# Kernel tuning notes

Hardware: AMD Instinct MI355X
Metric: run time of the kernel (lower is better)

## Reference

```python
import jax, jax.numpy as jnp
import numpy as np

K = 3
STRIDE = 1
PAD = 1
IN_CH = 64
OUT_CH = 128
ALPHA = 0.5  # scaling_factor
QMAX = 127.0  # 8-bit symmetric fake quant


def fake_quant(x):
    # per-tensor symmetric 8-bit fake quant with dynamic amax + STE
    amax = jnp.max(jnp.abs(jax.lax.stop_gradient(x)))
    s = jnp.where(amax > 0, amax / QMAX, 1.0)
    q = jnp.clip(jnp.round(x / s), -QMAX, QMAX) * s
    return x + jax.lax.stop_gradient(q - x)


def im2col(x, k, stride, pad):
    # x: (B, C, H, W) -> (B, C*k*k, h_out*w_out), torch.nn.functional.unfold order (C slowest, then kh, kw)
    B, C, H, W = x.shape
    h_out = (H + 2 * pad - k) // stride + 1
    w_out = (W + 2 * pad - k) // stride + 1
    xp = jnp.pad(x, ((0, 0), (0, 0), (pad, pad), (pad, pad)))
    patches = [xp[:, :, i:i + stride * h_out:stride, j:j + stride * w_out:stride]
               for i in range(k) for j in range(k)]  # fixed k*k loop
    cols = jnp.stack(patches, axis=2)  # (B, C, k*k, h_out, w_out)
    return cols.reshape(B, C * k * k, h_out * w_out), h_out, w_out


def setup_inputs() -> dict:
    key = jax.random.key(0)
    k1, k2 = jax.random.split(key)
    inp = jax.random.normal(k1, (16, IN_CH, 128, 128), dtype=jnp.float32)
    weight = jax.random.normal(k2, (OUT_CH, IN_CH, K, K), dtype=jnp.float32) * 0.05
    return {"input": inp, "weight": weight}


def reference(input, weight):
    bs = input.shape[0]
    ksize = IN_CH * K * K
    cols, h_out, w_out = im2col(input, K, STRIDE, PAD)  # (B, ksize, L)
    num_sliding = cols.shape[2]
    x = jnp.transpose(cols, (0, 2, 1)).reshape(-1, ksize)  # (B*L, ksize)
    w_flat = weight.reshape(OUT_CH, ksize)

    act_scale = jnp.max(jnp.abs(jax.lax.stop_gradient(x)), axis=0)       # (ksize,)
    weight_scale = jnp.max(jnp.abs(jax.lax.stop_gradient(w_flat)), axis=0)  # (ksize,)
    scale = act_scale ** ALPHA / weight_scale ** (1.0 - ALPHA)
    scale = jnp.where(scale == 0, 1.0, scale)

    x = fake_quant(x / scale)
    w_flat = fake_quant(w_flat * scale)

    out = jnp.einsum('nk,ok->no', x, w_flat)  # (B*L, OUT_CH)
    out = out.reshape(bs, num_sliding, OUT_CH)
    out = jnp.transpose(out, (0, 2, 1)).reshape(bs, OUT_CH, h_out, w_out)
    return out
```

## Files before the change

### kernel.cpp

```cpp
#include <hip/hip_runtime.h>

#define BATCH 16
#define CIN   64
#define HW    128
#define OC    128
#define KSIZE 576

typedef float float4v __attribute__((ext_vector_type(4)));
typedef int   int4v   __attribute__((ext_vector_type(4)));
typedef unsigned int uint;

#define WS_ACT   0
#define WS_WSC   576
#define WS_XMUL  1152
#define WS_SXSW  1728
#define WS_WQ_BYTE_OFF 8192

#define SWZ(x) ((((x) & 3) ^ (((x) >> 2) & 3)))
#define MAGIC 12582912.0f

__device__ __forceinline__ void async_cp16(const void* g, void* l) {
    __builtin_amdgcn_global_load_lds(
        (const __attribute__((address_space(1))) unsigned int*)g,
        (__attribute__((address_space(3))) unsigned int*)l, 16, 0, 0);
}

__global__ __launch_bounds__(256) void k_absmax(const float* __restrict__ in,
                                                const float* __restrict__ w,
                                                float* __restrict__ wsf) {
    const int tid = threadIdx.x, lane = tid & 63, wid = tid >> 6;
    if (blockIdx.x < 1024) {
        const int c = blockIdx.x >> 4, bs = blockIdx.x & 15;
        const float4v* p = (const float4v*)(in + (size_t)(bs * CIN + c) * (HW * HW));
        float m[9];
#pragma unroll
        for (int i = 0; i < 9; ++i) m[i] = 0.f;
        for (int e = tid; e < 4096; e += 256) {
            const int h = e >> 5, q = e & 31;
            const float4v v = p[e];
            const float a0 = fabsf(v[0]), a1 = fabsf(v[1]), a2 = fabsf(v[2]), a3 = fabsf(v[3]);
            const float m01 = fmaxf(a0, a1), m12 = fmaxf(a1, a2);
            const float mall = fmaxf(m01, fmaxf(a2, a3));
            const float mw0 = (q == 31) ? fmaxf(m01, a2) : mall;
            const float mw2 = (q == 0)  ? fmaxf(m12, a3) : mall;
            const bool h0 = (h <= 126), h2 = (h >= 1);
            m[0] = fmaxf(m[0], h0 ? mw0 : 0.f);
            m[1] = fmaxf(m[1], h0 ? mall : 0.f);
            m[2] = fmaxf(m[2], h0 ? mw2 : 0.f);
            m[3] = fmaxf(m[3], mw0);
            m[4] = fmaxf(m[4], mall);
            m[5] = fmaxf(m[5], mw2);
            m[6] = fmaxf(m[6], h2 ? mw0 : 0.f);
            m[7] = fmaxf(m[7], h2 ? mall : 0.f);
            m[8] = fmaxf(m[8], h2 ? mw2 : 0.f);
        }
#pragma unroll
        for (int i = 0; i < 9; ++i)
            for (int off = 32; off; off >>= 1)
                m[i] = fmaxf(m[i], __shfl_down(m[i], off));
        __shared__ float sred[4][9];
        if (lane == 0)
#pragma unroll
            for (int i = 0; i < 9; ++i) sred[wid][i] = m[i];
        __syncthreads();
        if (tid < 9) {
            float mm = fmaxf(fmaxf(sred[0][tid], sred[1][tid]),
                             fmaxf(sred[2][tid], sred[3][tid]));
            atomicMax((int*)(wsf + WS_ACT + c * 9 + tid), __float_as_int(mm));
        }
    } else {
        const int k = (blockIdx.x - 1024) * 4 + wid;
        float m = fmaxf(fabsf(w[lane * KSIZE + k]), fabsf(w[(lane + 64) * KSIZE + k]));
        for (int off = 32; off; off >>= 1) m = fmaxf(m, __shfl_down(m, off));
        if (lane == 0) wsf[WS_WSC + k] = m;
    }
}

__global__ __launch_bounds__(576) void k_scale_wq(const float* __restrict__ w,
                                                  float* __restrict__ wsf,
                                                  char* __restrict__ wq_s) {
    __shared__ float ls[576];
    __shared__ float redA[9], redB[9];
    const int t = threadIdx.x, o = blockIdx.x;
    const int lane = t & 63, wid = t >> 6;
    const float a = wsf[WS_ACT + t];
    const float wv = wsf[WS_WSC + t];
    float s = sqrtf(a) / sqrtf(wv);
    if (s == 0.f) s = 1.f;
    ls[t] = s;
    float v1 = a / s;
    float v2 = wv * s;
    for (int off = 32; off; off >>= 1) {
        v1 = fmaxf(v1, __shfl_down(v1, off));
        v2 = fmaxf(v2, __shfl_down(v2, off));
    }
    if (lane == 0) { redA[wid] = v1; redB[wid] = v2; }
    __syncthreads();
    float ax = redA[0], aw = redB[0];
#pragma unroll
    for (int i = 1; i < 9; ++i) { ax = fmaxf(ax, redA[i]); aw = fmaxf(aw, redB[i]); }
    const float sx = ax > 0.f ? ax / 127.f : 1.f;
    const float sw = aw > 0.f ? aw / 127.f : 1.f;
    const int r = t >> 6, c = t & 63, ko = c * 9 + r;
    float q = rintf((w[o * KSIZE + ko] * ls[ko]) / sw);
    q = fminf(127.f, fmaxf(-127.f, q));
    const int qi = (int)q;
    const int fc = c >> 4;
    wq_s[r * 8192 + o * 64 + ((fc ^ SWZ(o)) << 4) + (c & 15)] = (char)qi;
    if (o == 0) {
        wsf[WS_XMUL + t] = 1.0f / (ls[ko] * sx);
        if (t == 0) wsf[WS_SXSW] = sx * sw;
    }
}

__global__ __launch_bounds__(512, 4) void k_gemm(const float* __restrict__ in,
                                                 const char* __restrict__ wq_s,
                                                 const float* __restrict__ wsf,
                                                 float* __restrict__ out) {
    __shared__ int4v Bl4[4608];
    __shared__ float xml[576];
    char* Bl = (char*)Bl4;

    const int tid = threadIdx.x, lane = tid & 63, w = tid >> 6;
    const int xcd = blockIdx.x & 7, idx = blockIdx.x >> 3;
    const int ohp = idx & 7;
    const int b = idx >> 3;
    const int wh = w >> 2, wm = w & 3;
    const int oh = xcd * 16 + ohp * 2 + wh;
    const int l15 = lane & 15, fsel = lane >> 4;
    const int ow0 = wm * 32 + l15;

#pragma unroll
    for (int i = 0; i < 9; ++i)
        async_cp16(wq_s + i * 8192 + tid * 16, Bl + i * 8192 + tid * 16);
    if (tid < 144)
        ((float4v*)xml)[tid] = ((const float4v*)(wsf + WS_XMUL))[tid];
    __syncthreads();

    const float* pb = in + ((size_t)b * CIN + fsel * 16) * (HW * HW);

    int4v acc0[8], acc1[8];
#pragma unroll
    for (int nt = 0; nt < 8; ++nt) {
        acc0[nt] = (int4v){0, 0, 0, 0};
        acc1[nt] = (int4v){0, 0, 0, 0};
    }

#pragma unroll
    for (int r = 0; r < 9; ++r) {
        const int kh = r / 3, kw = r - 3 * kh;
        const int h = oh + kh - 1;
        if (h >= 0 && h < HW) {
            const int iw0 = ow0 + kw - 1;
            const int iw1 = iw0 + 16;
            int iwc0 = iw0, iwc1 = iw1;
            if (kw == 0) iwc0 = iw0 < 0 ? 0 : iw0;
            if (kw == 2) iwc1 = iw1 > 127 ? 127 : iw1;
            const float* p0 = pb + h * HW + iwc0;
            const float* p1 = pb + h * HW + iwc1;
            float v0[16], v1[16];
#pragma unroll
            for (int j = 0; j < 16; ++j) {
                v0[j] = p0[j * (HW * HW)];
                v1[j] = p1[j * (HW * HW)];
            }
            const float* xp = xml + r * 64 + (fsel << 4);
            uint pk0[4], pk1[4];
#pragma unroll
            for (int d = 0; d < 4; ++d) {
                const float4v xq = *(const float4v*)(xp + d * 4);
                uint u0[4], u1[4];
#pragma unroll
                for (int j2 = 0; j2 < 4; ++j2) {
                    u0[j2] = __float_as_uint(fmaf(v0[d * 4 + j2], xq[j2], MAGIC));
                    u1[j2] = __float_as_uint(fmaf(v1[d * 4 + j2], xq[j2], MAGIC));
                }
                const uint a01 = __builtin_amdgcn_perm(u0[1], u0[0], 0x0C0C0400u);
                const uint a23 = __builtin_amdgcn_perm(u0[3], u0[2], 0x0C0C0400u);
                pk0[d] = __builtin_amdgcn_perm(a23, a01, 0x05040100u);
                const uint b01 = __builtin_amdgcn_perm(u1[1], u1[0], 0x0C0C0400u);
                const uint b23 = __builtin_amdgcn_perm(u1[3], u1[2], 0x0C0C0400u);
                pk1[d] = __builtin_amdgcn_perm(b23, b01, 0x05040100u);
            }
            int4v af0, af1;
            if (kw == 0) {
                const uint msk = ((unsigned)iw0 < 128u) ? 0xFFFFFFFFu : 0u;
                af0 = (int4v){(int)(pk0[0] & msk), (int)(pk0[1] & msk),
                              (int)(pk0[2] & msk), (int)(pk0[3] & msk)};
                af1 = (int4v){(int)pk1[0], (int)pk1[1], (int)pk1[2], (int)pk1[3]};
            } else if (kw == 2) {
                const uint msk = ((unsigned)iw1 < 128u) ? 0xFFFFFFFFu : 0u;
                af0 = (int4v){(int)pk0[0], (int)pk0[1], (int)pk0[2], (int)pk0[3]};
                af1 = (int4v){(int)(pk1[0] & msk), (int)(pk1[1] & msk),
                              (int)(pk1[2] & msk), (int)(pk1[3] & msk)};
            } else {
                af0 = (int4v){(int)pk0[0], (int)pk0[1], (int)pk0[2], (int)pk0[3]};
                af1 = (int4v){(int)pk1[0], (int)pk1[1], (int)pk1[2], (int)pk1[3]};
            }
#pragma unroll
            for (int nt = 0; nt < 8; ++nt) {
                const int br = nt * 16 + l15;
                const int4v bf = *(const int4v*)(Bl + r * 8192 + br * 64 +
                                                 ((fsel ^ SWZ(br)) << 4));
                acc0[nt] = __builtin_amdgcn_mfma_i32_16x16x64_i8(af0, bf, acc0[nt], 0, 0, 0);
                acc1[nt] = __builtin_amdgcn_mfma_i32_16x16x64_i8(af1, bf, acc1[nt], 0, 0, 0);
            }
        }
    }

    const float sxsw = wsf[WS_SXSW];
    const int owp = wm * 32 + (fsel << 2);
#pragma unroll
    for (int nt = 0; nt < 8; ++nt) {
        const int o = nt * 16 + l15;
        float4v rv0, rv1;
#pragma unroll
        for (int q = 0; q < 4; ++q) {
            rv0[q] = (float)acc0[nt][q] * sxsw;
            rv1[q] = (float)acc1[nt][q] * sxsw;
        }
        float* po = out + ((size_t)(b * OC + o) * HW + oh) * HW;
        *(float4v*)(po + owp) = rv0;
        *(float4v*)(po + owp + 16) = rv1;
    }
}

extern "C" void kernel_launch(void* const* d_in, const int* in_sizes, int n_in,
                              void* d_out, int out_size, void* d_ws, size_t ws_size,
                              hipStream_t stream) {
    const float* in = (const float*)d_in[0];
    const float* wt = (const float*)d_in[1];
    float* out = (float*)d_out;
    float* wsf = (float*)d_ws;
    char* wq_s = (char*)d_ws + WS_WQ_BYTE_OFF;

    k_absmax<<<dim3(1024 + 144), dim3(256), 0, stream>>>(in, wt, wsf);
    k_scale_wq<<<dim3(128), dim3(576), 0, stream>>>(wt, wsf, wq_s);
    k_gemm<<<dim3(BATCH * HW / 2), dim3(512), 0, stream>>>(in, wq_s, wsf, out);
}
```

Before: 222.3 us.

## Build all activation fragments before the barrier, then run MFMAs per output-tile pair

The loop is restructured so that all nine kernel-position activation fragments are loaded, quantized and packed into registers first. The barrier moves after this phase, so the async weight-to-LDS copy overlaps with the global loads and quantization. MFMAs then run over output-channel pairs with a smaller accumulator set, and each pair's results are stored as soon as it finishes. Out-of-bounds rows are handled with clamped addresses plus masks instead of a branch, and the scale vector is read from global memory instead of LDS. Holding 18 fragment vectors raises register pressure, and edge rows now issue loads that are thrown away.

```diff
diff --git a/kernel.cpp b/kernel.cpp
--- a/kernel.cpp
+++ b/kernel.cpp
@@ -118,7 +118,6 @@
                                                  const float* __restrict__ wsf,
                                                  float* __restrict__ out) {
     __shared__ int4v Bl4[4608];
-    __shared__ float xml[576];
     char* Bl = (char*)Bl4;
 
     const int tid = threadIdx.x, lane = tid & 63, w = tid >> 6;
@@ -133,95 +132,92 @@
 #pragma unroll
     for (int i = 0; i < 9; ++i)
         async_cp16(wq_s + i * 8192 + tid * 16, Bl + i * 8192 + tid * 16);
-    if (tid < 144)
-        ((float4v*)xml)[tid] = ((const float4v*)(wsf + WS_XMUL))[tid];
-    __syncthreads();
 
     const float* pb = in + ((size_t)b * CIN + fsel * 16) * (HW * HW);
-
-    int4v acc0[8], acc1[8];
-#pragma unroll
-    for (int nt = 0; nt < 8; ++nt) {
-        acc0[nt] = (int4v){0, 0, 0, 0};
-        acc1[nt] = (int4v){0, 0, 0, 0};
-    }
-
+    const float* xmg = wsf + WS_XMUL;
+
+    int4v af0[9], af1[9];
 #pragma unroll
     for (int r = 0; r < 9; ++r) {
         const int kh = r / 3, kw = r - 3 * kh;
         const int h = oh + kh - 1;
-        if (h >= 0 && h < HW) {
-            const int iw0 = ow0 + kw - 1;
-            const int iw1 = iw0 + 16;
-            int iwc0 = iw0, iwc1 = iw1;
-            if (kw == 0) iwc0 = iw0 < 0 ? 0 : iw0;
-            if (kw == 2) iwc1 = iw1 > 127 ? 127 : iw1;
-            const float* p0 = pb + h * HW + iwc0;
-            const float* p1 = pb + h * HW + iwc1;
-            float v0[16], v1[16];
-#pragma unroll
-            for (int j = 0; j < 16; ++j) {
-                v0[j] = p0[j * (HW * HW)];
-                v1[j] = p1[j * (HW * HW)];
+        const int hc = h < 0 ? 0 : (h > 127 ? 127 : h);
+        const bool hok = (h >= 0) & (h < 128);
+        const int iw0 = ow0 + kw - 1;
+        const int iw1 = iw0 + 16;
+        int iwc0 = iw0, iwc1 = iw1;
+        if (kw == 0) iwc0 = iw0 < 0 ? 0 : iw0;
+        if (kw == 2) iwc1 = iw1 > 127 ? 127 : iw1;
+        const float* p0 = pb + hc * HW + iwc0;
+        const float* p1 = pb + hc * HW + iwc1;
+        float v0[16], v1[16];
+#pragma unroll
+        for (int j = 0; j < 16; ++j) {
+            v0[j] = p0[j * (HW * HW)];
+            v1[j] = p1[j * (HW * HW)];
+        }
+        uint pk0[4], pk1[4];
+#pragma unroll
+        for (int d = 0; d < 4; ++d) {
+            const float4v xq = *(const float4v*)(xmg + r * 64 + (fsel << 4) + d * 4);
+            uint u0[4], u1[4];
+#pragma unroll
+            for (int j2 = 0; j2 < 4; ++j2) {
+                u0[j2] = __float_as_uint(fmaf(v0[d * 4 + j2], xq[j2], MAGIC));
+                u1[j2] = __float_as_uint(fmaf(v1[d * 4 + j2], xq[j2], MAGIC));
             }
-            const float* xp = xml + r * 64 + (fsel << 4);
-            uint pk0[4], pk1[4];
-#pragma unroll
-            for (int d = 0; d < 4; ++d) {
-                const float4v xq = *(const float4v*)(xp + d * 4);
-                uint u0[4], u1[4];
-#pragma unroll
-                for (int j2 = 0; j2 < 4; ++j2) {
-                    u0[j2] = __float_as_uint(fmaf(v0[d * 4 + j2], xq[j2], MAGIC));
-                    u1[j2] = __float_as_uint(fmaf(v1[d * 4 + j2], xq[j2], MAGIC));
-                }
-                const uint a01 = __builtin_amdgcn_perm(u0[1], u0[0], 0x0C0C0400u);
-                const uint a23 = __builtin_amdgcn_perm(u0[3], u0[2], 0x0C0C0400u);
-                pk0[d] = __builtin_amdgcn_perm(a23, a01, 0x05040100u);
-                const uint b01 = __builtin_amdgcn_perm(u1[1], u1[0], 0x0C0C0400u);
-                const uint b23 = __builtin_amdgcn_perm(u1[3], u1[2], 0x0C0C0400u);
-                pk1[d] = __builtin_amdgcn_perm(b23, b01, 0x05040100u);
-            }
-            int4v af0, af1;
-            if (kw == 0) {
-                const uint msk = ((unsigned)iw0 < 128u) ? 0xFFFFFFFFu : 0u;
-                af0 = (int4v){(int)(pk0[0] & msk), (int)(pk0[1] & msk),
-                              (int)(pk0[2] & msk), (int)(pk0[3] & msk)};
-                af1 = (int4v){(int)pk1[0], (int)pk1[1], (int)pk1[2], (int)pk1[3]};
-            } else if (kw == 2) {
-                const uint msk = ((unsigned)iw1 < 128u) ? 0xFFFFFFFFu : 0u;
-                af0 = (int4v){(int)pk0[0], (int)pk0[1], (int)pk0[2], (int)pk0[3]};
-                af1 = (int4v){(int)(pk1[0] & msk), (int)(pk1[1] & msk),
-                              (int)(pk1[2] & msk), (int)(pk1[3] & msk)};
-            } else {
-                af0 = (int4v){(int)pk0[0], (int)pk0[1], (int)pk0[2], (int)pk0[3]};
-                af1 = (int4v){(int)pk1[0], (int)pk1[1], (int)pk1[2], (int)pk1[3]};
-            }
-#pragma unroll
-            for (int nt = 0; nt < 8; ++nt) {
-                const int br = nt * 16 + l15;
-                const int4v bf = *(const int4v*)(Bl + r * 8192 + br * 64 +
-                                                 ((fsel ^ SWZ(br)) << 4));
-                acc0[nt] = __builtin_amdgcn_mfma_i32_16x16x64_i8(af0, bf, acc0[nt], 0, 0, 0);
-                acc1[nt] = __builtin_amdgcn_mfma_i32_16x16x64_i8(af1, bf, acc1[nt], 0, 0, 0);
-            }
-        }
-    }
+            const uint a01 = __builtin_amdgcn_perm(u0[1], u0[0], 0x0C0C0400u);
+            const uint a23 = __builtin_amdgcn_perm(u0[3], u0[2], 0x0C0C0400u);
+            pk0[d] = __builtin_amdgcn_perm(a23, a01, 0x05040100u);
+            const uint b01 = __builtin_amdgcn_perm(u1[1], u1[0], 0x0C0C0400u);
+            const uint b23 = __builtin_amdgcn_perm(u1[3], u1[2], 0x0C0C0400u);
+            pk1[d] = __builtin_amdgcn_perm(b23, b01, 0x05040100u);
+        }
+        uint m0 = hok ? 0xFFFFFFFFu : 0u;
+        uint m1 = m0;
+        if (kw == 0) { if (!((unsigned)iw0 < 128u)) m0 = 0u; }
+        if (kw == 2) { if (!((unsigned)iw1 < 128u)) m1 = 0u; }
+        af0[r] = (int4v){(int)(pk0[0] & m0), (int)(pk0[1] & m0),
+                         (int)(pk0[2] & m0), (int)(pk0[3] & m0)};
+        af1[r] = (int4v){(int)(pk1[0] & m1), (int)(pk1[1] & m1),
+                         (int)(pk1[2] & m1), (int)(pk1[3] & m1)};
+    }
+
+    __syncthreads();
 
     const float sxsw = wsf[WS_SXSW];
     const int owp = wm * 32 + (fsel << 2);
 #pragma unroll
-    for (int nt = 0; nt < 8; ++nt) {
-        const int o = nt * 16 + l15;
-        float4v rv0, rv1;
-#pragma unroll
-        for (int q = 0; q < 4; ++q) {
-            rv0[q] = (float)acc0[nt][q] * sxsw;
-            rv1[q] = (float)acc1[nt][q] * sxsw;
-        }
-        float* po = out + ((size_t)(b * OC + o) * HW + oh) * HW;
-        *(float4v*)(po + owp) = rv0;
-        *(float4v*)(po + owp + 16) = rv1;
+    for (int p = 0; p < 4; ++p) {
+        int4v acc[4];
+#pragma unroll
+        for (int q = 0; q < 4; ++q) acc[q] = (int4v){0, 0, 0, 0};
+        const int br0 = (2 * p) * 16 + l15;
+        const int br1 = br0 + 16;
+        const int off0 = br0 * 64 + ((fsel ^ SWZ(br0)) << 4);
+        const int off1 = br1 * 64 + ((fsel ^ SWZ(br1)) << 4);
+#pragma unroll
+        for (int r = 0; r < 9; ++r) {
+            const int4v bf0 = *(const int4v*)(Bl + r * 8192 + off0);
+            const int4v bf1 = *(const int4v*)(Bl + r * 8192 + off1);
+            acc[0] = __builtin_amdgcn_mfma_i32_16x16x64_i8(af0[r], bf0, acc[0], 0, 0, 0);
+            acc[1] = __builtin_amdgcn_mfma_i32_16x16x64_i8(af1[r], bf0, acc[1], 0, 0, 0);
+            acc[2] = __builtin_amdgcn_mfma_i32_16x16x64_i8(af0[r], bf1, acc[2], 0, 0, 0);
+            acc[3] = __builtin_amdgcn_mfma_i32_16x16x64_i8(af1[r], bf1, acc[3], 0, 0, 0);
+        }
+#pragma unroll
+        for (int s = 0; s < 2; ++s) {
+            const int o = (2 * p + s) * 16 + l15;
+            float4v rv0, rv1;
+#pragma unroll
+            for (int q = 0; q < 4; ++q) {
+                rv0[q] = (float)acc[2 * s + 0][q] * sxsw;
+                rv1[q] = (float)acc[2 * s + 1][q] * sxsw;
+            }
+            float* po = out + ((size_t)(b * OC + o) * HW + oh) * HW;
+            *(float4v*)(po + owp) = rv0;
+            *(float4v*)(po + owp + 16) = rv1;
+        }
     }
 }
 
```

Result: slower. 250.9 us (+12.9%).

## Software-pipeline activation loads in conv GEMM with register double buffering

Applied to the files above, without the earlier changes.

Restructures the 9-tap loop into 18 half-chunks that prefetch the next tap's 16 activation values into a register buffer while the current half's MFMAs run, and issues the first prefetch before the barrier so it overlaps the async LDS weight copy. Out-of-range rows are now clamped and masked instead of skipped by a branch, so edge rows do extra zero MFMAs. This raises register pressure under the 512-thread, 4-blocks launch bound, which may cause spills.

```diff
diff --git a/kernel.cpp b/kernel.cpp
--- a/kernel.cpp
+++ b/kernel.cpp
@@ -113,6 +113,27 @@
     }
 }
 
+__device__ __forceinline__ const float* a_ptr(const float* pb, int oh, int ow0,
+                                              int R, int F) {
+    const int kh = R / 3, kw = R % 3;
+    int h = oh + kh - 1;
+    h = h < 0 ? 0 : (h > 127 ? 127 : h);
+    int iw = ow0 + (F ? 16 : 0) + kw - 1;
+    if (kw == 0 && F == 0) iw = iw < 0 ? 0 : iw;
+    if (kw == 2 && F == 1) iw = iw > 127 ? 127 : iw;
+    return pb + h * HW + iw;
+}
+
+__device__ __forceinline__ uint a_msk(int oh, int ow0, int R, int F) {
+    const int kh = R / 3, kw = R % 3;
+    const int h = oh + kh - 1;
+    uint m = ((unsigned)h < 128u) ? 0xFFFFFFFFu : 0u;
+    const int iw = ow0 + (F ? 16 : 0) + kw - 1;
+    if ((kw == 0 && F == 0) || (kw == 2 && F == 1))
+        if (!((unsigned)iw < 128u)) m = 0u;
+    return m;
+}
+
 __global__ __launch_bounds__(512, 4) void k_gemm(const float* __restrict__ in,
                                                  const char* __restrict__ wq_s,
                                                  const float* __restrict__ wsf,
@@ -135,9 +156,19 @@
         async_cp16(wq_s + i * 8192 + tid * 16, Bl + i * 8192 + tid * 16);
     if (tid < 144)
         ((float4v*)xml)[tid] = ((const float4v*)(wsf + WS_XMUL))[tid];
-    __syncthreads();
 
     const float* pb = in + ((size_t)b * CIN + fsel * 16) * (HW * HW);
+
+    float vbuf[2][16];
+    {
+        const float* p0 = a_ptr(pb, oh, ow0, 0, 0);
+        const float* p1 = a_ptr(pb, oh, ow0, 0, 1);
+#pragma unroll
+        for (int j = 0; j < 16; ++j) {
+            vbuf[0][j] = p0[j * (HW * HW)];
+            vbuf[1][j] = p1[j * (HW * HW)];
+        }
+    }
 
     int4v acc0[8], acc1[8];
 #pragma unroll
@@ -146,67 +177,58 @@
         acc1[nt] = (int4v){0, 0, 0, 0};
     }
 
-#pragma unroll
-    for (int r = 0; r < 9; ++r) {
-        const int kh = r / 3, kw = r - 3 * kh;
-        const int h = oh + kh - 1;
-        if (h >= 0 && h < HW) {
-            const int iw0 = ow0 + kw - 1;
-            const int iw1 = iw0 + 16;
-            int iwc0 = iw0, iwc1 = iw1;
-            if (kw == 0) iwc0 = iw0 < 0 ? 0 : iw0;
-            if (kw == 2) iwc1 = iw1 > 127 ? 127 : iw1;
-            const float* p0 = pb + h * HW + iwc0;
-            const float* p1 = pb + h * HW + iwc1;
-            float v0[16], v1[16];
-#pragma unroll
-            for (int j = 0; j < 16; ++j) {
-                v0[j] = p0[j * (HW * HW)];
-                v1[j] = p1[j * (HW * HW)];
-            }
-            const float* xp = xml + r * 64 + (fsel << 4);
-            uint pk0[4], pk1[4];
-#pragma unroll
-            for (int d = 0; d < 4; ++d) {
-                const float4v xq = *(const float4v*)(xp + d * 4);
-                uint u0[4], u1[4];
-#pragma unroll
-                for (int j2 = 0; j2 < 4; ++j2) {
-                    u0[j2] = __float_as_uint(fmaf(v0[d * 4 + j2], xq[j2], MAGIC));
-                    u1[j2] = __float_as_uint(fmaf(v1[d * 4 + j2], xq[j2], MAGIC));
-                }
-                const uint a01 = __builtin_amdgcn_perm(u0[1], u0[0], 0x0C0C0400u);
-                const uint a23 = __builtin_amdgcn_perm(u0[3], u0[2], 0x0C0C0400u);
-                pk0[d] = __builtin_amdgcn_perm(a23, a01, 0x05040100u);
-                const uint b01 = __builtin_amdgcn_perm(u1[1], u1[0], 0x0C0C0400u);
-                const uint b23 = __builtin_amdgcn_perm(u1[3], u1[2], 0x0C0C0400u);
-                pk1[d] = __builtin_amdgcn_perm(b23, b01, 0x05040100u);
-            }
-            int4v af0, af1;
-            if (kw == 0) {
-                const uint msk = ((unsigned)iw0 < 128u) ? 0xFFFFFFFFu : 0u;
-                af0 = (int4v){(int)(pk0[0] & msk), (int)(pk0[1] & msk),
-                              (int)(pk0[2] & msk), (int)(pk0[3] & msk)};
-                af1 = (int4v){(int)pk1[0], (int)pk1[1], (int)pk1[2], (int)pk1[3]};
-            } else if (kw == 2) {
-                const uint msk = ((unsigned)iw1 < 128u) ? 0xFFFFFFFFu : 0u;
-                af0 = (int4v){(int)pk0[0], (int)pk0[1], (int)pk0[2], (int)pk0[3]};
-                af1 = (int4v){(int)(pk1[0] & msk), (int)(pk1[1] & msk),
-                              (int)(pk1[2] & msk), (int)(pk1[3] & msk)};
-            } else {
-                af0 = (int4v){(int)pk0[0], (int)pk0[1], (int)pk0[2], (int)pk0[3]};
-                af1 = (int4v){(int)pk1[0], (int)pk1[1], (int)pk1[2], (int)pk1[3]};
-            }
-#pragma unroll
-            for (int nt = 0; nt < 8; ++nt) {
-                const int br = nt * 16 + l15;
-                const int4v bf = *(const int4v*)(Bl + r * 8192 + br * 64 +
-                                                 ((fsel ^ SWZ(br)) << 4));
-                acc0[nt] = __builtin_amdgcn_mfma_i32_16x16x64_i8(af0, bf, acc0[nt], 0, 0, 0);
-                acc1[nt] = __builtin_amdgcn_mfma_i32_16x16x64_i8(af1, bf, acc1[nt], 0, 0, 0);
-            }
-        }
-    }
+    __syncthreads();
+
+#define HALFCHUNK(HC)                                                          \
+    {                                                                          \
+        constexpr int R = (HC) >> 1, F = (HC) & 1;                             \
+        const float* xp = xml + R * 64 + (fsel << 4);                          \
+        uint pk[4];                                                            \
+        _Pragma("unroll")                                                      \
+        for (int d = 0; d < 4; ++d) {                                          \
+            const float4v xq = *(const float4v*)(xp + d * 4);                  \
+            uint u[4];                                                         \
+            _Pragma("unroll")                                                  \
+            for (int j2 = 0; j2 < 4; ++j2)                                     \
+                u[j2] = __float_as_uint(fmaf(vbuf[F][d * 4 + j2], xq[j2], MAGIC)); \
+            const uint p01 = __builtin_amdgcn_perm(u[1], u[0], 0x0C0C0400u);   \
+            const uint p23 = __builtin_amdgcn_perm(u[3], u[2], 0x0C0C0400u);   \
+            pk[d] = __builtin_amdgcn_perm(p23, p01, 0x05040100u);              \
+        }                                                                      \
+        const uint msk = a_msk(oh, ow0, R, F);                                 \
+        const int4v af = (int4v){(int)(pk[0] & msk), (int)(pk[1] & msk),       \
+                                 (int)(pk[2] & msk), (int)(pk[3] & msk)};      \
+        if ((HC) + 2 < 18) {                                                   \
+            const float* pn = a_ptr(pb, oh, ow0, ((HC) + 2) >> 1, F);          \
+            _Pragma("unroll")                                                  \
+            for (int j = 0; j < 16; ++j) vbuf[F][j] = pn[j * (HW * HW)];       \
+        }                                                                      \
+        if (F == 0) {                                                          \
+            _Pragma("unroll")                                                  \
+            for (int nt = 0; nt < 8; ++nt) {                                   \
+                const int br = nt * 16 + l15;                                  \
+                const int4v bf = *(const int4v*)(Bl + R * 8192 + br * 64 +     \
+                                                 ((fsel ^ SWZ(br)) << 4));     \
+                acc0[nt] = __builtin_amdgcn_mfma_i32_16x16x64_i8(af, bf,       \
+                                                          acc0[nt], 0, 0, 0); \
+            }                                                                  \
+        } else {                                                               \
+            _Pragma("unroll")                                                  \
+            for (int nt = 0; nt < 8; ++nt) {                                   \
+                const int br = nt * 16 + l15;                                  \
+                const int4v bf = *(const int4v*)(Bl + R * 8192 + br * 64 +     \
+                                                 ((fsel ^ SWZ(br)) << 4));     \
+                acc1[nt] = __builtin_amdgcn_mfma_i32_16x16x64_i8(af, bf,       \
+                                                          acc1[nt], 0, 0, 0); \
+            }                                                                  \
+        }                                                                      \
+    }
+
+    HALFCHUNK(0)  HALFCHUNK(1)  HALFCHUNK(2)  HALFCHUNK(3)  HALFCHUNK(4)
+    HALFCHUNK(5)  HALFCHUNK(6)  HALFCHUNK(7)  HALFCHUNK(8)  HALFCHUNK(9)
+    HALFCHUNK(10) HALFCHUNK(11) HALFCHUNK(12) HALFCHUNK(13) HALFCHUNK(14)
+    HALFCHUNK(15) HALFCHUNK(16) HALFCHUNK(17)
+#undef HALFCHUNK
 
     const float sxsw = wsf[WS_SXSW];
     const int owp = wm * 32 + (fsel << 2);
```

Measured after the change: 437.8 us. 1.97x slower.

## Load each input row once per kh and derive kw shifts via lane shuffles

Applied to the files above, without the earlier changes.

The GEMM kernel now loads the 32 input columns for each kernel row once and builds the left and right shifted tap operands with cross-lane shuffles inside 16-lane groups. Halo columns come from a separate per-lane load that is broadcast with shuffles. This cuts global/L2 loads by about a factor of three. In exchange it adds many shuffle (ds_bpermute/DPP) instructions and selects per element, which could raise VALU/LDS pressure and register use.

```diff
diff --git a/kernel.cpp b/kernel.cpp
--- a/kernel.cpp
+++ b/kernel.cpp
@@ -128,7 +128,7 @@
     const int wh = w >> 2, wm = w & 3;
     const int oh = xcd * 16 + ohp * 2 + wh;
     const int l15 = lane & 15, fsel = lane >> 4;
-    const int ow0 = wm * 32 + l15;
+    const int W = wm * 32;
 
 #pragma unroll
     for (int i = 0; i < 9; ++i)
@@ -138,6 +138,14 @@
     __syncthreads();
 
     const float* pb = in + ((size_t)b * CIN + fsel * 16) * (HW * HW);
+    const float* pe = in + (size_t)b * CIN * (HW * HW);
+
+    const int colL = (W - 1) < 0 ? 0 : (W - 1);
+    const int colR = (W + 32) > 127 ? 127 : (W + 32);
+    const bool isL0  = (l15 == 0);
+    const bool isL15 = (l15 == 15);
+    const uint mL = (wm == 0 && isL0)  ? 0u : 0xFFFFFFFFu;
+    const uint mR = (wm == 3 && isL15) ? 0u : 0xFFFFFFFFu;
 
     int4v acc0[8], acc1[8];
 #pragma unroll
@@ -147,69 +155,86 @@
     }
 
 #pragma unroll
-    for (int r = 0; r < 9; ++r) {
-        const int kh = r / 3, kw = r - 3 * kh;
+    for (int kh = 0; kh < 3; ++kh) {
         const int h = oh + kh - 1;
         if (h >= 0 && h < HW) {
-            const int iw0 = ow0 + kw - 1;
-            const int iw1 = iw0 + 16;
-            int iwc0 = iw0, iwc1 = iw1;
-            if (kw == 0) iwc0 = iw0 < 0 ? 0 : iw0;
-            if (kw == 2) iwc1 = iw1 > 127 ? 127 : iw1;
-            const float* p0 = pb + h * HW + iwc0;
-            const float* p1 = pb + h * HW + iwc1;
-            float v0[16], v1[16];
+            const float eL = pe[(size_t)lane * (HW * HW) + h * HW + colL];
+            const float eR = pe[(size_t)lane * (HW * HW) + h * HW + colR];
+            const float* p = pb + h * HW + W + l15;
+            float R0[16], R1[16];
 #pragma unroll
             for (int j = 0; j < 16; ++j) {
-                v0[j] = p0[j * (HW * HW)];
-                v1[j] = p1[j * (HW * HW)];
+                R0[j] = p[j * (HW * HW)];
+                R1[j] = p[j * (HW * HW) + 16];
             }
-            const float* xp = xml + r * 64 + (fsel << 4);
-            uint pk0[4], pk1[4];
-#pragma unroll
-            for (int d = 0; d < 4; ++d) {
-                const float4v xq = *(const float4v*)(xp + d * 4);
-                uint u0[4], u1[4];
-#pragma unroll
-                for (int j2 = 0; j2 < 4; ++j2) {
-                    u0[j2] = __float_as_uint(fmaf(v0[d * 4 + j2], xq[j2], MAGIC));
-                    u1[j2] = __float_as_uint(fmaf(v1[d * 4 + j2], xq[j2], MAGIC));
+#pragma unroll
+            for (int kw = 0; kw < 3; ++kw) {
+                const int r = kh * 3 + kw;
+                const float* xp = xml + r * 64 + (fsel << 4);
+                uint pk0[4], pk1[4];
+#pragma unroll
+                for (int d = 0; d < 4; ++d) {
+                    const float4v xq = *(const float4v*)(xp + d * 4);
+                    uint u0[4], u1[4];
+#pragma unroll
+                    for (int j2 = 0; j2 < 4; ++j2) {
+                        const int j = d * 4 + j2;
+                        float a0, a1;
+                        if (kw == 1) {
+                            a0 = R0[j];
+                            a1 = R1[j];
+                        } else if (kw == 0) {
+                            const float t0 = __shfl_up(R0[j], 1, 16);
+                            const float ev = __shfl(eL, j, 16);
+                            a0 = isL0 ? ev : t0;
+                            const float t1 = __shfl_up(R1[j], 1, 16);
+                            const float bb = __shfl(R0[j], 15, 16);
+                            a1 = isL0 ? bb : t1;
+                        } else {
+                            const float t0 = __shfl_down(R0[j], 1, 16);
+                            const float bb = __shfl(R1[j], 0, 16);
+                            a0 = isL15 ? bb : t0;
+                            const float t1 = __shfl_down(R1[j], 1, 16);
+                            const float ev = __shfl(eR, j, 16);
+                            a1 = isL15 ? ev : t1;
+                        }
+                        u0[j2] = __float_as_uint(fmaf(a0, xq[j2], MAGIC));
+                        u1[j2] = __float_as_uint(fmaf(a1, xq[j2], MAGIC));
+                    }
+                    const uint a01 = __builtin_amdgcn_perm(u0[1], u0[0], 0x0C0C0400u);
+                    const uint a23 = __builtin_amdgcn_perm(u0[3], u0[2], 0x0C0C0400u);
+                    pk0[d] = __builtin_amdgcn_perm(a23, a01, 0x05040100u);
+                    const uint b01 = __builtin_amdgcn_perm(u1[1], u1[0], 0x0C0C0400u);
+                    const uint b23 = __builtin_amdgcn_perm(u1[3], u1[2], 0x0C0C0400u);
+                    pk1[d] = __builtin_amdgcn_perm(b23, b01, 0x05040100u);
                 }
-                const uint a01 = __builtin_amdgcn_perm(u0[1], u0[0], 0x0C0C0400u);
-                const uint a23 = __builtin_amdgcn_perm(u0[3], u0[2], 0x0C0C0400u);
-                pk0[d] = __builtin_amdgcn_perm(a23, a01, 0x05040100u);
-                const uint b01 = __builtin_amdgcn_perm(u1[1], u1[0], 0x0C0C0400u);
-                const uint b23 = __builtin_amdgcn_perm(u1[3], u1[2], 0x0C0C0400u);
-                pk1[d] = __builtin_amdgcn_perm(b23, b01, 0x05040100u);
+                int4v af0, af1;
+                if (kw == 0) {
+                    af0 = (int4v){(int)(pk0[0] & mL), (int)(pk0[1] & mL),
+                                  (int)(pk0[2] & mL), (int)(pk0[3] & mL)};
+                    af1 = (int4v){(int)pk1[0], (int)pk1[1], (int)pk1[2], (int)pk1[3]};
+                } else if (kw == 2) {
+                    af0 = (int4v){(int)pk0[0], (int)pk0[1], (int)pk0[2], (int)pk0[3]};
+                    af1 = (int4v){(int)(pk1[0] & mR), (int)(pk1[1] & mR),
+                                  (int)(pk1[2] & mR), (int)(pk1[3] & mR)};
+                } else {
+                    af0 = (int4v){(int)pk0[0], (int)pk0[1], (int)pk0[2], (int)pk0[3]};
+                    af1 = (int4v){(int)pk1[0], (int)pk1[1], (int)pk1[2], (int)pk1[3]};
+                }
+#pragma unroll
+                for (int nt = 0; nt < 8; ++nt) {
+                    const int br = nt * 16 + l15;
+                    const int4v bf = *(const int4v*)(Bl + r * 8192 + br * 64 +
+                                                     ((fsel ^ SWZ(br)) << 4));
+                    acc0[nt] = __builtin_amdgcn_mfma_i32_16x16x64_i8(af0, bf, acc0[nt], 0, 0, 0);
+                    acc1[nt] = __builtin_amdgcn_mfma_i32_16x16x64_i8(af1, bf, acc1[nt], 0, 0, 0);
+                }
             }
-            int4v af0, af1;
-            if (kw == 0) {
-                const uint msk = ((unsigned)iw0 < 128u) ? 0xFFFFFFFFu : 0u;
-                af0 = (int4v){(int)(pk0[0] & msk), (int)(pk0[1] & msk),
-                              (int)(pk0[2] & msk), (int)(pk0[3] & msk)};
-                af1 = (int4v){(int)pk1[0], (int)pk1[1], (int)pk1[2], (int)pk1[3]};
-            } else if (kw == 2) {
-                const uint msk = ((unsigned)iw1 < 128u) ? 0xFFFFFFFFu : 0u;
-                af0 = (int4v){(int)pk0[0], (int)pk0[1], (int)pk0[2], (int)pk0[3]};
-                af1 = (int4v){(int)(pk1[0] & msk), (int)(pk1[1] & msk),
-                              (int)(pk1[2] & msk), (int)(pk1[3] & msk)};
-            } else {
-                af0 = (int4v){(int)pk0[0], (int)pk0[1], (int)pk0[2], (int)pk0[3]};
-                af1 = (int4v){(int)pk1[0], (int)pk1[1], (int)pk1[2], (int)pk1[3]};
-            }
-#pragma unroll
-            for (int nt = 0; nt < 8; ++nt) {
-                const int br = nt * 16 + l15;
-                const int4v bf = *(const int4v*)(Bl + r * 8192 + br * 64 +
-                                                 ((fsel ^ SWZ(br)) << 4));
-                acc0[nt] = __builtin_amdgcn_mfma_i32_16x16x64_i8(af0, bf, acc0[nt], 0, 0, 0);
-                acc1[nt] = __builtin_amdgcn_mfma_i32_16x16x64_i8(af1, bf, acc1[nt], 0, 0, 0);
-            }
         }
     }
 
     const float sxsw = wsf[WS_SXSW];
-    const int owp = wm * 32 + (fsel << 2);
+    const int owp = W + (fsel << 2);
 #pragma unroll
     for (int nt = 0; nt < 8; ++nt) {
         const int o = nt * 16 + l15;
```

Result: slower. 278.1 us (+25.1%).
